# Kernel tuning notes

Measured on AMD Instinct MI355X. Metric: run time of the kernel, lower is better.

Reference implementation:

```python
import jax, jax.numpy as jnp
import numpy as np

SCALE = 8
NUM_CLASSES = 15
IGNORE_THRES = 0.5
# anchors for scale=8 divided by scale
GRID_ANCHOR = jnp.array([[96.0 / 8, 230.0 / 8], [79.0 / 8, 186.0 / 8], [81.0 / 8, 133.0 / 8]], dtype=jnp.float32)  # [3,2]


def _bce_sum(p, t, mask):
    # torch BCELoss(reduction='sum') with log clamped at -100, restricted to mask
    lp = jnp.maximum(jnp.log(p), -100.0)
    ln = jnp.maximum(jnp.log(1.0 - p), -100.0)
    return jnp.sum(-(t * lp + (1.0 - t) * ln) * mask)


def setup_inputs() -> dict:
    key = jax.random.key(0)
    k1, k2, k3 = jax.random.split(key, 3)
    nB, nG = 128, 52
    x = jax.random.normal(k1, (nB, 3 * (NUM_CLASSES + 5), nG, nG), dtype=jnp.float32)
    boxes = jax.random.uniform(k2, (nB, 4), minval=0.1, maxval=0.6)  # cx,cy,w,h in (0,1)
    cls = jax.random.randint(k3, (nB, 1), 0, NUM_CLASSES).astype(jnp.float32)
    labels = jnp.concatenate([boxes, cls], axis=-1)  # [nB,5]
    return {"x": x, "labels": labels}


def reference(x, labels):
    nB, nG = x.shape[0], x.shape[2]
    pred = x.reshape(nB, 3, NUM_CLASSES + 5, nG, nG).transpose(0, 1, 3, 4, 2)  # [B,3,G,G,20]
    px = jax.nn.sigmoid(pred[..., 0])
    py = jax.nn.sigmoid(pred[..., 1])
    pw = pred[..., 2]
    ph = pred[..., 3]
    conf = jax.nn.sigmoid(pred[..., 4])
    cls = jax.nn.softmax(pred[..., 5:], axis=-1)
    pred_boxs = jnp.stack([px, py, pw, ph], axis=-1)  # [B,3,G,G,4]
    out = jnp.concatenate([
        pred_boxs.reshape(nB, -1, 4) * SCALE,
        conf.reshape(nB, -1, 1),
        cls.reshape(nB, -1, NUM_CLASSES),
    ], axis=-1)

    # ---- build_targets (vectorized; one target per image as in original loop) ----
    tb = labels[:, :4] * nG  # boxes in grid units [B,4]
    gx, gy, gw, gh = tb[:, 0], tb[:, 1], tb[:, 2], tb[:, 3]
    gi = gx.astype(jnp.int32)
    gj = gy.astype(jnp.int32)
    gcls = labels[:, 4].astype(jnp.int32)

    # wh-IoU anchors vs targets -> [3,B]
    aw, ah = GRID_ANCHOR[:, 0:1], GRID_ANCHOR[:, 1:2]
    inter_wh = jnp.minimum(aw, gw[None, :]) * jnp.minimum(ah, gh[None, :])
    ious = inter_wh / (aw * ah + 1e-16 + gw[None, :] * gh[None, :] - inter_wh)
    best_idx = jnp.argmax(ious, axis=0)  # [B]

    bidx = jnp.arange(nB)
    shape4 = (nB, 3, nG, nG)
    obj = jnp.zeros(shape4, jnp.float32).at[bidx, best_idx, gj, gi].set(1.0)

    noobj = jnp.ones(shape4, jnp.float32)
    arep = jnp.tile(jnp.arange(3), nB)
    brep = jnp.repeat(bidx, 3)
    jrep = jnp.repeat(gj, 3)
    irep = jnp.repeat(gi, 3)
    ign = (jnp.reshape(ious.T, (-1,)) > IGNORE_THRES).astype(jnp.float32)
    noobj = noobj.at[brep, arep, jrep, irep].mul(1.0 - ign)
    noobj = noobj.at[bidx, best_idx, gj, gi].set(0.0)

    gif = gi.astype(jnp.float32)
    gjf = gj.astype(jnp.float32)
    tx = jnp.zeros(shape4, jnp.float32).at[bidx, best_idx, gj, gi].set(gx - gif)
    ty = jnp.zeros(shape4, jnp.float32).at[bidx, best_idx, gj, gi].set(gy - gjf)
    tw = jnp.zeros(shape4, jnp.float32).at[bidx, best_idx, gj, gi].set(jnp.log(gw / GRID_ANCHOR[best_idx, 0] + 1e-16))
    th = jnp.zeros(shape4, jnp.float32).at[bidx, best_idx, gj, gi].set(jnp.log(gh / GRID_ANCHOR[best_idx, 1] + 1e-16))
    tcls = jnp.zeros(shape4 + (NUM_CLASSES,), jnp.float32).at[bidx, best_idx, gj, gi, gcls].set(1.0)

    # cls_mask: does argmax of predicted class at target cell match gt class
    pred_cls_at = cls[bidx, best_idx, gj, gi]  # [B,15]
    cls_hit = (jnp.argmax(pred_cls_at, axis=-1) == gcls).astype(jnp.float32)
    cls_mask = jnp.zeros(shape4, jnp.float32).at[bidx, best_idx, gj, gi].set(cls_hit)

    # iou between pred box at target cell and target box (cxcywh, +1 corner convention)
    pb = pred_boxs[bidx, best_idx, gj, gi]  # [B,4]
    b1x1, b1y1 = pb[:, 0] - pb[:, 2] / 2, pb[:, 1] - pb[:, 3] / 2
    b1x2, b1y2 = pb[:, 0] + pb[:, 2] / 2, pb[:, 1] + pb[:, 3] / 2
    b2x1, b2y1 = gx - gw / 2, gy - gh / 2
    b2x2, b2y2 = gx + gw / 2, gy + gh / 2
    iw = jnp.clip(jnp.minimum(b1x2, b2x2) - jnp.maximum(b1x1, b2x1) + 1, 0)
    ih = jnp.clip(jnp.minimum(b1y2, b2y2) - jnp.maximum(b1y1, b2y1) + 1, 0)
    inter = iw * ih
    a1 = (b1x2 - b1x1 + 1) * (b1y2 - b1y1 + 1)
    a2 = (b2x2 - b2x1 + 1) * (b2y2 - b2y1 + 1)
    iou_vec = inter / (a1 + a2 - inter + 1e-16)
    iou_scores = jnp.zeros(shape4, jnp.float32).at[bidx, best_idx, gj, gi].set(iou_vec)

    tconf = obj
    # ---- losses (boolean-mask indexing replaced by masked sums) ----
    loss_x = jnp.sum(jnp.abs(px - tx) * obj)
    loss_y = jnp.sum(jnp.abs(py - ty) * obj)
    loss_w = jnp.sum(jnp.abs(pw - tw) * obj)
    loss_h = jnp.sum(jnp.abs(ph - th) * obj)
    loss_conf = _bce_sum(conf, tconf, obj) + 100.0 * _bce_sum(conf, tconf, noobj)
    loss_cls = _bce_sum(cls, tcls, obj[..., None])
    loss = loss_x + loss_y + loss_w + loss_h + loss_conf + loss_cls
    return (loss, out)
```

## Files before the change

kernel.cpp:

```cpp
#include <hip/hip_runtime.h>
#include <math.h>

#define NB    128
#define NG    52
#define NGG   2704
#define NA    3
#define NCLS  15
#define NCH   20
#define TOTAL 1038336
#define PLANES (NB*NA)
#define WVP   43
#define NSLOT (PLANES*WVP)
#define WPB   4
#define BLK   256
#define NBLK2 (NSLOT/WPB)
#define FPW   (64*NCH)
#define NPART NSLOT

typedef float f4 __attribute__((ext_vector_type(4)));

__device__ __forceinline__ void gload_lds(const float* g, float* l) {
    __builtin_amdgcn_global_load_lds(
        (const __attribute__((address_space(1))) void*)g,
        (__attribute__((address_space(3))) void*)l, 4, 0, 0);
}

__global__ __launch_bounds__(BLK) void main_kernel(const float* __restrict__ x,
                                                   const float* __restrict__ labels,
                                                   float* __restrict__ out,
                                                   float* __restrict__ partials) {
    __shared__ __align__(16) float sm[WPB][FPW];

    int t = threadIdx.x;
    int w = t >> 6;
    int l = t & 63;
    int wslot = blockIdx.x * WPB + w;
    int p  = wslot / WVP;
    int k  = wslot - p * WVP;
    int b  = p / 3;
    int a  = p - b * 3;
    int ji0 = k * 64;
    int ji  = ji0 + l;
    bool active = (ji < NGG);
    int NACT = (NGG - ji0 < 64) ? (NGG - ji0) : 64;
    int FACT = NACT * NCH;

    float* __restrict__ smw = sm[w];
    const float* __restrict__ xplane = x + ((size_t)(b*60 + a*20)) * NGG + ji0;

    if (active) {
        #pragma unroll
        for (int c = 0; c < NCH; c++)
            gload_lds(xplane + c * NGG + l, &smw[c * 64]);
    }
    asm volatile("s_waitcnt vmcnt(0)" ::: "memory");
    __builtin_amdgcn_sched_barrier(0);

    float z[NCH];
    #pragma unroll
    for (int c = 0; c < NCH; c++) z[c] = smw[c * 64 + l];

    float v[NCH];
    float conf = 1.0f / (1.0f + __expf(-z[4]));
    v[0] = 8.0f / (1.0f + __expf(-z[0]));
    v[1] = 8.0f / (1.0f + __expf(-z[1]));
    v[2] = 8.0f * z[2];
    v[3] = 8.0f * z[3];
    v[4] = conf;
    float m = z[5];
    #pragma unroll
    for (int c = 6; c < NCH; c++) m = fmaxf(m, z[c]);
    float s = 0.0f;
    #pragma unroll
    for (int c = 0; c < NCLS; c++) { v[5+c] = __expf(z[5+c] - m); s += v[5+c]; }
    float inv = 1.0f / s;
    #pragma unroll
    for (int c = 0; c < NCLS; c++) v[5+c] *= inv;

    float gx = labels[b*5+0] * (float)NG;
    float gy = labels[b*5+1] * (float)NG;
    float gw = labels[b*5+2] * (float)NG;
    float gh = labels[b*5+3] * (float)NG;
    int  gcls = (int)labels[b*5+4];
    int gi = (int)gx, gj = (int)gy;
    float gwgh = gw * gh;
    float i0 = fminf(12.0f,   gw) * fminf(28.75f,  gh);
    float i1 = fminf(9.875f,  gw) * fminf(23.25f,  gh);
    float i2 = fminf(10.125f, gw) * fminf(16.625f, gh);
    float iou0 = i0 / (345.0f      + 1e-16f + gwgh - i0);
    float iou1 = i1 / (229.59375f  + 1e-16f + gwgh - i1);
    float iou2 = i2 / (168.328125f + 1e-16f + gwgh - i2);
    int best = 0; float bv = iou0;
    if (iou1 > bv) { best = 1; bv = iou1; }
    if (iou2 > bv) { best = 2; bv = iou2; }
    float ioua = (a == 0) ? iou0 : ((a == 1) ? iou1 : iou2);
    bool at_t   = (ji == gj * NG + gi);
    bool isbest = (a == best);

    float tsum = 0.0f;
    if (active) {
        if (!(at_t && (isbest || ioua > 0.5f)))
            tsum = -100.0f * fmaxf(__logf(1.0f - conf), -100.0f);
        if (at_t && isbest) {
            tsum += -fmaxf(__logf(conf), -100.0f);
            float txv = gx - (float)gi;
            float tyv = gy - (float)gj;
            float abw = (best == 0) ? 12.0f  : ((best == 1) ? 9.875f : 10.125f);
            float abh = (best == 0) ? 28.75f : ((best == 1) ? 23.25f : 16.625f);
            float twv = __logf(gw / abw + 1e-16f);
            float thv = __logf(gh / abh + 1e-16f);
            tsum += fabsf(v[0]*0.125f - txv) + fabsf(v[1]*0.125f - tyv)
                  + fabsf(v[2]*0.125f - twv) + fabsf(v[3]*0.125f - thv);
            #pragma unroll
            for (int c = 0; c < NCLS; c++) {
                float pc = v[5+c];
                tsum += (c == gcls) ? -fmaxf(__logf(pc),        -100.0f)
                                    : -fmaxf(__logf(1.0f - pc), -100.0f);
            }
        }
    }

    asm volatile("s_waitcnt lgkmcnt(0)" ::: "memory");
    if (active) {
        int base = l * NCH - 3;
        #pragma unroll
        for (int c = 0; c < NCH; c++) {
            int L = base + c;
            if (L < 0) L += FPW;
            smw[L] = v[c];
        }
    }

    #pragma unroll
    for (int off = 32; off > 0; off >>= 1) tsum += __shfl_down(tsum, off, 64);

    int NQ4w = (FACT - 4) / 4;
    int cell0 = p * NGG + ji0;
    size_t gf = 1 + (size_t)cell0 * NCH;
    f4* __restrict__ op = (f4*)(out + gf + 3);
    const f4* __restrict__ sp = (const f4*)smw;
    #pragma unroll
    for (int kk = 0; kk < 5; kk++) {
        int q = kk * 64 + l;
        if (q < NQ4w) op[q] = sp[q];
    }
    if (l == 0) {
        out[gf + 0]        = smw[FPW - 3];
        out[gf + 1]        = smw[FPW - 2];
        out[gf + 2]        = smw[FPW - 1];
        out[gf + FACT - 1] = smw[FACT - 4];
        partials[wslot] = tsum;
    }
}

__global__ __launch_bounds__(1024) void finish_kernel(const float* __restrict__ partials,
                                                      float* __restrict__ out) {
    int t = threadIdx.x;
    float s = 0.0f;
    #pragma unroll
    for (int k = 0; k < NPART/1024 + 1; k++) {
        int q = k * 1024 + t;
        if (q < NPART) s += partials[q];
    }
    __shared__ float red[1024];
    red[t] = s;
    __syncthreads();
    for (int k = 512; k > 0; k >>= 1) {
        if (t < k) red[t] += red[t + k];
        __syncthreads();
    }
    if (t == 0) out[0] = red[0];
}

extern "C" void kernel_launch(void* const* d_in, const int* in_sizes, int n_in,
                              void* d_out, int out_size, void* d_ws, size_t ws_size,
                              hipStream_t stream) {
    const float* x      = (const float*)d_in[0];
    const float* labels = (const float*)d_in[1];
    float* out = (float*)d_out;
    float* ws  = (float*)d_ws;

    hipLaunchKernelGGL(main_kernel,   dim3(NBLK2), dim3(BLK),  0, stream, x, labels, out, ws);
    hipLaunchKernelGGL(finish_kernel, dim3(1),     dim3(1024), 0, stream, ws, out);
}
```

Before: 152.0 us.

## Make waves persistent over 8 chunks with double-buffered async LDS loads

Each wave now processes eight consecutive 64-cell chunks instead of one. Global-to-LDS loads are double-buffered, so the next chunk's loads are in flight while the current chunk is computed and stored. Partial sums accumulate across chunks, which cuts the partial count and the final reduction work. In exchange the grid is eight times smaller, which lowers the number of resident waves available to hide latency, and the hand-set vmcnt values depend on exact counts of outstanding loads and stores.

```diff
diff --git a/kernel.cpp b/kernel.cpp
--- a/kernel.cpp
+++ b/kernel.cpp
@@ -7,15 +7,16 @@
 #define NA    3
 #define NCLS  15
 #define NCH   20
-#define TOTAL 1038336
 #define PLANES (NB*NA)
 #define WVP   43
 #define NSLOT (PLANES*WVP)
+#define ITERS 8
+#define NWAVE (NSLOT/ITERS)
 #define WPB   4
 #define BLK   256
-#define NBLK2 (NSLOT/WPB)
+#define NBLK3 (NWAVE/WPB)
 #define FPW   (64*NCH)
-#define NPART NSLOT
+#define NPART NWAVE
 
 typedef float f4 __attribute__((ext_vector_type(4)));
 
@@ -25,40 +26,38 @@
         (__attribute__((address_space(3))) void*)l, 4, 0, 0);
 }
 
-__global__ __launch_bounds__(BLK) void main_kernel(const float* __restrict__ x,
-                                                   const float* __restrict__ labels,
-                                                   float* __restrict__ out,
-                                                   float* __restrict__ partials) {
-    __shared__ __align__(16) float sm[WPB][FPW];
-
-    int t = threadIdx.x;
-    int w = t >> 6;
-    int l = t & 63;
-    int wslot = blockIdx.x * WPB + w;
-    int p  = wslot / WVP;
-    int k  = wslot - p * WVP;
-    int b  = p / 3;
-    int a  = p - b * 3;
+__device__ __forceinline__ void stage_chunk(const float* __restrict__ x,
+                                            int chunk, int l, float* buf) {
+    int p   = chunk / WVP;
+    int k   = chunk - p * WVP;
+    int ji0 = k * 64;
+    bool active = (ji0 + l < NGG);
+    const float* g = x + (size_t)p * (NCH * NGG) + ji0 + l;
+    if (active) {
+        #pragma unroll
+        for (int c = 0; c < NCH; c++)
+            gload_lds(g + c * NGG, buf + c * 64);
+    }
+}
+
+__device__ __forceinline__ void process_chunk(const float* __restrict__ labels,
+                                              float* __restrict__ out,
+                                              int chunk, int l,
+                                              float* __restrict__ buf,
+                                              float& tsum) {
+    int p   = chunk / WVP;
+    int k   = chunk - p * WVP;
+    int b   = p / 3;
+    int a   = p - b * 3;
     int ji0 = k * 64;
     int ji  = ji0 + l;
     bool active = (ji < NGG);
     int NACT = (NGG - ji0 < 64) ? (NGG - ji0) : 64;
     int FACT = NACT * NCH;
 
-    float* __restrict__ smw = sm[w];
-    const float* __restrict__ xplane = x + ((size_t)(b*60 + a*20)) * NGG + ji0;
-
-    if (active) {
-        #pragma unroll
-        for (int c = 0; c < NCH; c++)
-            gload_lds(xplane + c * NGG + l, &smw[c * 64]);
-    }
-    asm volatile("s_waitcnt vmcnt(0)" ::: "memory");
-    __builtin_amdgcn_sched_barrier(0);
-
     float z[NCH];
     #pragma unroll
-    for (int c = 0; c < NCH; c++) z[c] = smw[c * 64 + l];
+    for (int c = 0; c < NCH; c++) z[c] = buf[c * 64 + l];
 
     float v[NCH];
     float conf = 1.0f / (1.0f + __expf(-z[4]));
@@ -97,10 +96,9 @@
     bool at_t   = (ji == gj * NG + gi);
     bool isbest = (a == best);
 
-    float tsum = 0.0f;
     if (active) {
         if (!(at_t && (isbest || ioua > 0.5f)))
-            tsum = -100.0f * fmaxf(__logf(1.0f - conf), -100.0f);
+            tsum += -100.0f * fmaxf(__logf(1.0f - conf), -100.0f);
         if (at_t && isbest) {
             tsum += -fmaxf(__logf(conf), -100.0f);
             float txv = gx - (float)gi;
@@ -127,30 +125,68 @@
         for (int c = 0; c < NCH; c++) {
             int L = base + c;
             if (L < 0) L += FPW;
-            smw[L] = v[c];
+            buf[L] = v[c];
         }
     }
-
-    #pragma unroll
-    for (int off = 32; off > 0; off >>= 1) tsum += __shfl_down(tsum, off, 64);
 
     int NQ4w = (FACT - 4) / 4;
     int cell0 = p * NGG + ji0;
     size_t gf = 1 + (size_t)cell0 * NCH;
     f4* __restrict__ op = (f4*)(out + gf + 3);
-    const f4* __restrict__ sp = (const f4*)smw;
+    const f4* __restrict__ sp = (const f4*)buf;
     #pragma unroll
     for (int kk = 0; kk < 5; kk++) {
         int q = kk * 64 + l;
         if (q < NQ4w) op[q] = sp[q];
     }
     if (l == 0) {
-        out[gf + 0]        = smw[FPW - 3];
-        out[gf + 1]        = smw[FPW - 2];
-        out[gf + 2]        = smw[FPW - 1];
-        out[gf + FACT - 1] = smw[FACT - 4];
-        partials[wslot] = tsum;
-    }
+        out[gf + 0]        = buf[FPW - 3];
+        out[gf + 1]        = buf[FPW - 2];
+        out[gf + 2]        = buf[FPW - 1];
+        out[gf + FACT - 1] = buf[FACT - 4];
+    }
+}
+
+#define WAIT_VMCNT(n) do {                                         \
+        asm volatile("s_waitcnt vmcnt(" #n ")" ::: "memory");      \
+        __builtin_amdgcn_sched_barrier(0);                         \
+    } while (0)
+
+__global__ __launch_bounds__(BLK) void main_kernel(const float* __restrict__ x,
+                                                   const float* __restrict__ labels,
+                                                   float* __restrict__ out,
+                                                   float* __restrict__ partials) {
+    __shared__ __align__(16) float sm[WPB][2][FPW];
+
+    int t = threadIdx.x;
+    int w = t >> 6;
+    int l = t & 63;
+    int wid   = blockIdx.x * WPB + w;
+    int slot0 = wid * ITERS;
+    float* __restrict__ b0 = &sm[w][0][0];
+    float* __restrict__ b1 = &sm[w][1][0];
+    float tsum = 0.0f;
+
+    stage_chunk(x, slot0 + 0, l, b0);
+    stage_chunk(x, slot0 + 1, l, b1);
+    WAIT_VMCNT(20);
+    process_chunk(labels, out, slot0 + 0, l, b0, tsum);
+
+    #pragma unroll
+    for (int it = 1; it < ITERS - 1; ++it) {
+        float* cur = (it & 1) ? b1 : b0;
+        float* nxt = (it & 1) ? b0 : b1;
+        stage_chunk(x, slot0 + it + 1, l, nxt);
+        WAIT_VMCNT(26);
+        process_chunk(labels, out, slot0 + it, l, cur, tsum);
+    }
+
+    WAIT_VMCNT(6);
+    process_chunk(labels, out, slot0 + ITERS - 1, l, b1, tsum);
+
+    #pragma unroll
+    for (int off = 32; off > 0; off >>= 1) tsum += __shfl_down(tsum, off, 64);
+    if (l == 0) partials[wid] = tsum;
 }
 
 __global__ __launch_bounds__(1024) void finish_kernel(const float* __restrict__ partials,
@@ -180,6 +216,6 @@
     float* out = (float*)d_out;
     float* ws  = (float*)d_ws;
 
-    hipLaunchKernelGGL(main_kernel,   dim3(NBLK2), dim3(BLK),  0, stream, x, labels, out, ws);
+    hipLaunchKernelGGL(main_kernel,   dim3(NBLK3), dim3(BLK),  0, stream, x, labels, out, ws);
     hipLaunchKernelGGL(finish_kernel, dim3(1),     dim3(1024), 0, stream, ws, out);
 }
```

Result: slower. 164.5 us (+8.2%).
